# Kernel tuning notes

Measured on AMD Instinct MI355X. Metric: run time of the kernel, lower is better.

The kernel has to match this reference:

```python
import jax, jax.numpy as jnp
import numpy as np

B, T, C, H = 8, 2048, 1024, 64


def setup_inputs() -> dict:
    key = jax.random.key(0)
    kx, kq, kk, kv = jax.random.split(key, 4)
    sc = 1.0 / np.sqrt(C)
    return {
        "x": jax.random.normal(kx, (B, T, C), dtype=jnp.float32),
        "Wq": jax.random.normal(kq, (C, H), dtype=jnp.float32) * sc,
        "Wk": jax.random.normal(kk, (C, H), dtype=jnp.float32) * sc,
        "Wv": jax.random.normal(kv, (C, H), dtype=jnp.float32) * sc,
    }


def reference(x, Wq, Wk, Wv):
    # Projections: Linear(C, head_size, bias=False) == x @ W
    q = jnp.einsum("btc,ch->bth", x, Wq)
    k = jnp.einsum("btc,ch->bth", x, Wk)
    v = jnp.einsum("btc,ch->bth", x, Wv)
    head_size = q.shape[-1]
    scale = head_size ** -0.5
    # scores: [B, T, T]
    scores = jnp.einsum("bqh,bkh->bqk", q, k) * scale
    # causal mask (tril==0 -> -inf)
    causal = jnp.tril(jnp.ones((scores.shape[1], scores.shape[2]), dtype=bool))
    scores = jnp.where(causal, scores, -jnp.inf)
    w = jax.nn.softmax(scores, axis=-1)
    # dropout_rate=0.0 -> identity
    out = jnp.einsum("bqk,bkh->bqh", w, v)
    return out
```

## Files before the change

### kernel.cpp

```cpp
#include <hip/hip_runtime.h>
#include <hip/hip_bf16.h>
#include <cstdint>
#include <cstddef>

typedef short bf16x8 __attribute__((ext_vector_type(8)));
typedef float f32x4 __attribute__((ext_vector_type(4)));

#define BN 8
#define TN 2048
#define CN 1024
#define HN 64

__device__ __forceinline__ unsigned short f2bf(float f) {
    unsigned int u = __float_as_uint(f);
    u += 0x7fffu + ((u >> 16) & 1u);
    return (unsigned short)(u >> 16);
}

__device__ __forceinline__ int pk2(float lo, float hi) {
    float2 t; t.x = lo; t.y = hi;
    __hip_bfloat162 h = __float22bfloat162_rn(t);
    return *reinterpret_cast<int*>(&h);
}

__device__ __forceinline__ void gload_lds16(const unsigned short* gsrc, void* ldst) {
    __builtin_amdgcn_global_load_lds(
        (const __attribute__((address_space(1))) unsigned int*)gsrc,
        (__attribute__((address_space(3))) unsigned int*)ldst,
        16, 0, 0);
}

__global__ __launch_bounds__(256) void wconv_kernel(const float* __restrict__ Wq,
                                                    const float* __restrict__ Wk,
                                                    const float* __restrict__ Wv,
                                                    unsigned short* __restrict__ Wp) {
    int idx = blockIdx.x * 256 + threadIdx.x;
    int n = idx >> 10;
    int c = idx & 1023;
    int m = n >> 6;
    int h = n & 63;
    const float* W = (m == 0) ? Wq : ((m == 1) ? Wk : Wv);
    float v = W[c * 64 + h];
    if (m == 0) v *= 0.18033688011112042f;
    const int tile = n >> 4, lq = n & 15;
    const int kk = c >> 5, lg = (c >> 3) & 3, e = c & 7;
    Wp[(size_t)(((tile * 32 + kk) * 64 + lg * 16 + lq) * 8 + e)] = f2bf(v);
}

__global__ __launch_bounds__(512) void proj_kernel(const float* __restrict__ X,
                                                   const unsigned short* __restrict__ Wp,
                                                   unsigned short* __restrict__ Qs,
                                                   unsigned short* __restrict__ Kp,
                                                   unsigned short* __restrict__ Vp) {
    __shared__ short Xs[2][64 * 64];
    __shared__ short Wsh[2][6144];

    const int tid = threadIdx.x;
    const int w   = tid >> 6;
    const int l   = tid & 63;
    const int lq  = l & 15;
    const int lg  = l >> 4;
    const int mr   = w >> 1;
    const int nsub = w & 1;
    const int bid = blockIdx.x;
    const int mtile = bid & 255;
    const int nh    = bid >> 8;
    const int rowbase = mtile * 64;

    const int xrow = tid >> 3;
    const int xcol = (tid & 7) * 8;
    const float* xsrc = X + (size_t)(rowbase + xrow) * CN + xcol;
    const int xdst = xrow * 128 + (((xcol * 2)) ^ ((xrow & 7) << 4));

    const unsigned short* wsrc0 = Wp + (size_t)((nh * 6 + (w >> 1)) * 32 + (w & 1)) * 512 + l * 8;
    const int wdstb0 = (w * 512) * 2;
    const unsigned short* wsrc1 = Wp + (size_t)((nh * 6 + 4 + (w >> 1)) * 32 + (w & 1)) * 512 + l * 8;
    const int wdstb1 = (4096 + w * 512) * 2;

    const int arow = mr * 16 + lq;
    int aaddr[2];
    #pragma unroll
    for (int kkL = 0; kkL < 2; ++kkL)
        aaddr[kkL] = arow * 128 + (((kkL * 64 + lg * 16)) ^ ((arow & 7) << 4));
    int baddr[2][3];
    #pragma unroll
    for (int kkL = 0; kkL < 2; ++kkL)
        #pragma unroll
        for (int jj = 0; jj < 3; ++jj)
            baddr[kkL][jj] = (((nsub * 3 + jj) * 2 + kkL) * 512 + l * 8) * 2;

    const f32x4 zero4 = {0.f, 0.f, 0.f, 0.f};
    f32x4 acc[3] = {zero4, zero4, zero4};

    {
        gload_lds16(wsrc0, (char*)Wsh[0] + wdstb0);
        if (tid < 256) gload_lds16(wsrc1, (char*)Wsh[0] + wdstb1);
        float4 xa = *(const float4*)(xsrc);
        float4 xb = *(const float4*)(xsrc + 4);
        int4 xc;
        xc.x = pk2(xa.x, xa.y); xc.y = pk2(xa.z, xa.w);
        xc.z = pk2(xb.x, xb.y); xc.w = pk2(xb.z, xb.w);
        *(int4*)((char*)Xs[0] + xdst) = xc;
        __syncthreads();
    }

    for (int s = 0; s < 16; ++s) {
        const int cur = s & 1;
        const int nxt = cur ^ 1;
        const bool more = (s + 1) < 16;
        float4 xa, xb;
        if (more) {
            xa = *(const float4*)(xsrc + (s + 1) * 64);
            xb = *(const float4*)(xsrc + (s + 1) * 64 + 4);
            gload_lds16(wsrc0 + (s + 1) * 1024, (char*)Wsh[nxt] + wdstb0);
            if (tid < 256) gload_lds16(wsrc1 + (s + 1) * 1024, (char*)Wsh[nxt] + wdstb1);
        }
        #pragma unroll
        for (int kkL = 0; kkL < 2; ++kkL) {
            bf16x8 a  = *(const bf16x8*)((char*)Xs[cur] + aaddr[kkL]);
            bf16x8 b0 = *(const bf16x8*)((char*)Wsh[cur] + baddr[kkL][0]);
            bf16x8 b1 = *(const bf16x8*)((char*)Wsh[cur] + baddr[kkL][1]);
            bf16x8 b2 = *(const bf16x8*)((char*)Wsh[cur] + baddr[kkL][2]);
            acc[0] = __builtin_amdgcn_mfma_f32_16x16x32_bf16(a, b0, acc[0], 0, 0, 0);
            acc[1] = __builtin_amdgcn_mfma_f32_16x16x32_bf16(a, b1, acc[1], 0, 0, 0);
            acc[2] = __builtin_amdgcn_mfma_f32_16x16x32_bf16(a, b2, acc[2], 0, 0, 0);
        }
        if (more) {
            int4 xc;
            xc.x = pk2(xa.x, xa.y); xc.y = pk2(xa.z, xa.w);
            xc.z = pk2(xb.x, xb.y); xc.w = pk2(xb.z, xb.w);
            *(int4*)((char*)Xs[nxt] + xdst) = xc;
        }
        __syncthreads();
    }

    #pragma unroll
    for (int jj = 0; jj < 3; ++jj) {
        const int col = nh * 96 + nsub * 48 + jj * 16 + lq;
        const int mtx = col >> 6;
        const int h   = col & 63;
        #pragma unroll
        for (int i = 0; i < 4; ++i) {
            const int g = rowbase + mr * 16 + 4 * lg + i;
            const unsigned short val = f2bf(acc[jj][i]);
            const int b = g >> 11, tloc = g & 2047;
            const int kt = tloc >> 5;
            if (mtx == 0) {
                Qs[(size_t)g * 64 + h] = val;
            } else if (mtx == 1) {
                const int fa = (tloc >> 4) & 1, lqk = tloc & 15;
                const int ks = h >> 5, lgk = (h >> 3) & 3, e = h & 7;
                Kp[(size_t)(b * 64 + kt) * 2048 + (fa * 2 + ks) * 512 +
                   (lgk * 16 + lqk) * 8 + e] = val;
            } else {
                const int tt = tloc & 31;
                const int lgv = (tt & 15) >> 2;
                const int e = (tt < 16) ? (tt & 3) : 4 + (tt & 3);
                const int nf = h >> 4, lqv = h & 15;
                Vp[(size_t)(b * 64 + kt) * 2048 + nf * 512 +
                   (lgv * 16 + lqv) * 8 + e] = val;
            }
        }
    }
}

__global__ __launch_bounds__(256) void attn_kernel(const unsigned short* __restrict__ Qs,
                                                   const unsigned short* __restrict__ Kp,
                                                   const unsigned short* __restrict__ Vp,
                                                   float* __restrict__ Out) {
    __shared__ float lm[4][16];
    __shared__ float ll[4][16];
    __shared__ float facc[4][1024];

    const int tid = threadIdx.x;
    const int w  = tid >> 6;
    const int l  = tid & 63;
    const int lq = l & 15;
    const int lg = l >> 4;
    const int bid = blockIdx.x;
    const int qt = 127 - (bid >> 3);
    const int b  = bid & 7;
    const int q0 = qt * 16;
    const int nt = (qt >> 1) + 1;

    const unsigned short* Qb = Qs + (size_t)b * TN * 64;
    const unsigned short* KVbase_k = Kp + (size_t)b * 64 * 2048 + (size_t)l * 8;
    const unsigned short* KVbase_v = Vp + (size_t)b * 64 * 2048 + (size_t)l * 8;

    const f32x4 zero4 = {0.f, 0.f, 0.f, 0.f};

    bf16x8 qa0 = *(const bf16x8*)(Qb + (size_t)(q0 + lq) * 64 + lg * 8);
    bf16x8 qa1 = *(const bf16x8*)(Qb + (size_t)(q0 + lq) * 64 + 32 + lg * 8);

    f32x4 acc[4] = {zero4, zero4, zero4, zero4};
    float mrow = -1e30f;
    float lrow = 0.f;

    bf16x8 Kc[4], Vc[4], Kn[4], Vn[4];
    int kt = w;
    if (kt < nt) {
        const size_t tb = (size_t)kt * 2048;
        #pragma unroll
        for (int i = 0; i < 4; ++i) {
            Kc[i] = *(const bf16x8*)(KVbase_k + tb + i * 512);
            Vc[i] = *(const bf16x8*)(KVbase_v + tb + i * 512);
        }
    }

    for (; kt < nt; kt += 4) {
        const int ktn = kt + 4;
        if (ktn < nt) {
            const size_t tb = (size_t)ktn * 2048;
            #pragma unroll
            for (int i = 0; i < 4; ++i) {
                Kn[i] = *(const bf16x8*)(KVbase_k + tb + i * 512);
                Vn[i] = *(const bf16x8*)(KVbase_v + tb + i * 512);
            }
        }

        const int key0 = kt * 32;
        f32x4 s[2];
        s[0] = __builtin_amdgcn_mfma_f32_16x16x32_bf16(Kc[0], qa0, zero4, 0, 0, 0);
        s[0] = __builtin_amdgcn_mfma_f32_16x16x32_bf16(Kc[1], qa1, s[0], 0, 0, 0);
        s[1] = __builtin_amdgcn_mfma_f32_16x16x32_bf16(Kc[2], qa0, zero4, 0, 0, 0);
        s[1] = __builtin_amdgcn_mfma_f32_16x16x32_bf16(Kc[3], qa1, s[1], 0, 0, 0);

        if (kt == nt - 1) {
            const int q = q0 + lq;
            #pragma unroll
            for (int fa = 0; fa < 2; ++fa)
                #pragma unroll
                for (int r = 0; r < 4; ++r) {
                    const int key = key0 + fa * 16 + 4 * lg + r;
                    if (key > q) s[fa][r] = -1e30f;
                }
        }

        float m1 = fmaxf(fmaxf(s[0][0], s[0][1]), s[0][2]);
        float m2 = fmaxf(fmaxf(s[0][3], s[1][0]), s[1][1]);
        float m3 = fmaxf(fmaxf(s[1][2], s[1][3]), m1);
        float tm = fmaxf(m2, m3);
        tm = fmaxf(tm, __shfl_xor(tm, 16));
        tm = fmaxf(tm, __shfl_xor(tm, 32));

        if (!__all(tm <= mrow + 8.0f)) {
            const float mnew = fmaxf(mrow, tm);
            const float cc = __builtin_amdgcn_exp2f(mrow - mnew);
            lrow *= cc;
            float cb[4];
            #pragma unroll
            for (int i = 0; i < 4; ++i) cb[i] = __shfl(cc, 4 * lg + i);
            #pragma unroll
            for (int nf = 0; nf < 4; ++nf)
                #pragma unroll
                for (int i = 0; i < 4; ++i) acc[nf][i] *= cb[i];
            mrow = mnew;
        }

        float p[2][4];
        float psum = 0.f;
        #pragma unroll
        for (int fa = 0; fa < 2; ++fa)
            #pragma unroll
            for (int r = 0; r < 4; ++r) {
                p[fa][r] = __builtin_amdgcn_exp2f(s[fa][r] - mrow);
                psum += p[fa][r];
            }
        psum += __shfl_xor(psum, 16);
        psum += __shfl_xor(psum, 32);
        lrow += psum;

        bf16x8 pa;
        pa[0] = (short)f2bf(p[0][0]); pa[1] = (short)f2bf(p[0][1]);
        pa[2] = (short)f2bf(p[0][2]); pa[3] = (short)f2bf(p[0][3]);
        pa[4] = (short)f2bf(p[1][0]); pa[5] = (short)f2bf(p[1][1]);
        pa[6] = (short)f2bf(p[1][2]); pa[7] = (short)f2bf(p[1][3]);

        acc[0] = __builtin_amdgcn_mfma_f32_16x16x32_bf16(pa, Vc[0], acc[0], 0, 0, 0);
        acc[1] = __builtin_amdgcn_mfma_f32_16x16x32_bf16(pa, Vc[1], acc[1], 0, 0, 0);
        acc[2] = __builtin_amdgcn_mfma_f32_16x16x32_bf16(pa, Vc[2], acc[2], 0, 0, 0);
        acc[3] = __builtin_amdgcn_mfma_f32_16x16x32_bf16(pa, Vc[3], acc[3], 0, 0, 0);

        #pragma unroll
        for (int i = 0; i < 4; ++i) { Kc[i] = Kn[i]; Vc[i] = Vn[i]; }
    }

    if (lg == 0) {
        lm[w][lq] = mrow;
        ll[w][lq] = lrow;
    }
    #pragma unroll
    for (int nf = 0; nf < 4; ++nf)
        #pragma unroll
        for (int i = 0; i < 4; ++i)
            facc[w][(4 * lg + i) * 64 + nf * 16 + lq] = acc[nf][i];

    __syncthreads();

    #pragma unroll
    for (int ii = 0; ii < 4; ++ii) {
        const int e = tid + ii * 256;
        const int q = e >> 6;
        const int h = e & 63;
        const float M = fmaxf(fmaxf(lm[0][q], lm[1][q]),
                              fmaxf(lm[2][q], lm[3][q]));
        float L = 0.f, O = 0.f;
        #pragma unroll
        for (int c = 0; c < 4; ++c) {
            const float wgt = __builtin_amdgcn_exp2f(lm[c][q] - M);
            L += wgt * ll[c][q];
            O += wgt * facc[c][q * 64 + h];
        }
        Out[((size_t)b * TN + q0 + q) * 64 + h] = O / L;
    }
}

extern "C" void kernel_launch(void* const* d_in, const int* in_sizes, int n_in,
                              void* d_out, int out_size, void* d_ws, size_t ws_size,
                              hipStream_t stream) {
    const float* X  = (const float*)d_in[0];
    const float* Wq = (const float*)d_in[1];
    const float* Wk = (const float*)d_in[2];
    const float* Wv = (const float*)d_in[3];
    float* Out = (float*)d_out;

    char* ws = (char*)d_ws;
    unsigned short* Wp = (unsigned short*)(ws);
    unsigned short* Qs = (unsigned short*)(ws + (512u << 10));
    unsigned short* Kp = Qs + (size_t)16384 * 64;
    unsigned short* Vp = Kp + (size_t)16384 * 64;

    hipLaunchKernelGGL(wconv_kernel, dim3(768), dim3(256), 0, stream, Wq, Wk, Wv, Wp);
    hipLaunchKernelGGL(proj_kernel,  dim3(512), dim3(512), 0, stream, X, Wp, Qs, Kp, Vp);
    hipLaunchKernelGGL(attn_kernel,  dim3(1024), dim3(256), 0, stream, Qs, Kp, Vp, Out);
}
```

Before: 43.25 us.

## Switch projection GEMM to 32x32x16 MFMA with six-wave 32x32 tiles

Measured after the change: 43.38 us. No clear change (+0.3%).

```diff
diff --git a/kernel.cpp b/kernel.cpp
--- a/kernel.cpp
+++ b/kernel.cpp
@@ -5,6 +5,7 @@
 
 typedef short bf16x8 __attribute__((ext_vector_type(8)));
 typedef float f32x4 __attribute__((ext_vector_type(4)));
+typedef float f32x16 __attribute__((ext_vector_type(16)));
 
 #define BN 8
 #define TN 2048
@@ -42,65 +43,77 @@
     const float* W = (m == 0) ? Wq : ((m == 1) ? Wk : Wv);
     float v = W[c * 64 + h];
     if (m == 0) v *= 0.18033688011112042f;
-    const int tile = n >> 4, lq = n & 15;
-    const int kk = c >> 5, lg = (c >> 3) & 3, e = c & 7;
-    Wp[(size_t)(((tile * 32 + kk) * 64 + lg * 16 + lq) * 8 + e)] = f2bf(v);
-}
-
-__global__ __launch_bounds__(512) void proj_kernel(const float* __restrict__ X,
+    const int tc = n >> 5, col = n & 31;
+    const int kk16 = c >> 4, khalf = (c >> 3) & 1, e = c & 7;
+    const int l = col + 32 * khalf;
+    Wp[(size_t)(((tc * 64 + kk16) * 64 + l) * 8 + e)] = f2bf(v);
+}
+
+__global__ __launch_bounds__(384) void proj_kernel(const float* __restrict__ X,
                                                    const unsigned short* __restrict__ Wp,
                                                    unsigned short* __restrict__ Qs,
                                                    unsigned short* __restrict__ Kp,
                                                    unsigned short* __restrict__ Vp) {
-    __shared__ short Xs[2][64 * 64];
+    __shared__ short Xs[2][4096];
     __shared__ short Wsh[2][6144];
 
     const int tid = threadIdx.x;
     const int w   = tid >> 6;
     const int l   = tid & 63;
-    const int lq  = l & 15;
-    const int lg  = l >> 4;
-    const int mr   = w >> 1;
-    const int nsub = w & 1;
+    const int m   = w / 3;
+    const int ntL = w % 3;
     const int bid = blockIdx.x;
     const int mtile = bid & 255;
     const int nh    = bid >> 8;
     const int rowbase = mtile * 64;
 
-    const int xrow = tid >> 3;
-    const int xcol = (tid & 7) * 8;
-    const float* xsrc = X + (size_t)(rowbase + xrow) * CN + xcol;
-    const int xdst = xrow * 128 + (((xcol * 2)) ^ ((xrow & 7) << 4));
-
-    const unsigned short* wsrc0 = Wp + (size_t)((nh * 6 + (w >> 1)) * 32 + (w & 1)) * 512 + l * 8;
-    const int wdstb0 = (w * 512) * 2;
-    const unsigned short* wsrc1 = Wp + (size_t)((nh * 6 + 4 + (w >> 1)) * 32 + (w & 1)) * 512 + l * 8;
-    const int wdstb1 = (4096 + w * 512) * 2;
-
-    const int arow = mr * 16 + lq;
-    int aaddr[2];
-    #pragma unroll
-    for (int kkL = 0; kkL < 2; ++kkL)
-        aaddr[kkL] = arow * 128 + (((kkL * 64 + lg * 16)) ^ ((arow & 7) << 4));
-    int baddr[2][3];
-    #pragma unroll
-    for (int kkL = 0; kkL < 2; ++kkL)
-        #pragma unroll
-        for (int jj = 0; jj < 3; ++jj)
-            baddr[kkL][jj] = (((nsub * 3 + jj) * 2 + kkL) * 512 + l * 8) * 2;
-
-    const f32x4 zero4 = {0.f, 0.f, 0.f, 0.f};
-    f32x4 acc[3] = {zero4, zero4, zero4};
+    const int r0 = tid >> 3;
+    const float* xsrc0 = X + (size_t)(rowbase + r0) * CN + (tid & 7) * 8;
+    const int xdst0 = r0 * 128 + (((tid & 7) * 16) ^ ((r0 & 7) << 4));
+    const int u1 = tid + 384;
+    const int r1 = u1 >> 3;
+    const float* xsrc1 = X + (size_t)(rowbase + r1) * CN + (u1 & 7) * 8;
+    const int xdst1 = r1 * 128 + (((u1 & 7) * 16) ^ ((r1 & 7) << 4));
+    const bool st2 = (tid < 128);
+
+    const unsigned short* wsrc[2];
+    int wdst[2];
+    #pragma unroll
+    for (int i = 0; i < 2; ++i) {
+        const int c = 2 * w + i;
+        const int tcL = c >> 2, kkL = c & 3;
+        wsrc[i] = Wp + (size_t)((nh * 3 + tcL) * 64 + kkL) * 512 + l * 8;
+        wdst[i] = c * 1024;
+    }
+
+    int aaddr[4], baddr[4];
+    #pragma unroll
+    for (int j = 0; j < 4; ++j) {
+        aaddr[j] = (m * 32 + (l & 31)) * 128 +
+                   ((j * 32 + (l >> 5) * 16) ^ ((l & 7) << 4));
+        baddr[j] = (ntL * 4 + j) * 1024 + l * 16;
+    }
+
+    f32x16 acc = {0.f, 0.f, 0.f, 0.f, 0.f, 0.f, 0.f, 0.f,
+                  0.f, 0.f, 0.f, 0.f, 0.f, 0.f, 0.f, 0.f};
 
     {
-        gload_lds16(wsrc0, (char*)Wsh[0] + wdstb0);
-        if (tid < 256) gload_lds16(wsrc1, (char*)Wsh[0] + wdstb1);
-        float4 xa = *(const float4*)(xsrc);
-        float4 xb = *(const float4*)(xsrc + 4);
+        gload_lds16(wsrc[0], (char*)Wsh[0] + wdst[0]);
+        gload_lds16(wsrc[1], (char*)Wsh[0] + wdst[1]);
+        float4 xa = *(const float4*)(xsrc0);
+        float4 xb = *(const float4*)(xsrc0 + 4);
         int4 xc;
         xc.x = pk2(xa.x, xa.y); xc.y = pk2(xa.z, xa.w);
         xc.z = pk2(xb.x, xb.y); xc.w = pk2(xb.z, xb.w);
-        *(int4*)((char*)Xs[0] + xdst) = xc;
+        *(int4*)((char*)Xs[0] + xdst0) = xc;
+        if (st2) {
+            float4 ya = *(const float4*)(xsrc1);
+            float4 yb = *(const float4*)(xsrc1 + 4);
+            int4 yc;
+            yc.x = pk2(ya.x, ya.y); yc.y = pk2(ya.z, ya.w);
+            yc.z = pk2(yb.x, yb.y); yc.w = pk2(yb.z, yb.w);
+            *(int4*)((char*)Xs[0] + xdst1) = yc;
+        }
         __syncthreads();
     }
 
@@ -108,58 +121,62 @@
         const int cur = s & 1;
         const int nxt = cur ^ 1;
         const bool more = (s + 1) < 16;
-        float4 xa, xb;
+        float4 xa, xb, ya, yb;
         if (more) {
-            xa = *(const float4*)(xsrc + (s + 1) * 64);
-            xb = *(const float4*)(xsrc + (s + 1) * 64 + 4);
-            gload_lds16(wsrc0 + (s + 1) * 1024, (char*)Wsh[nxt] + wdstb0);
-            if (tid < 256) gload_lds16(wsrc1 + (s + 1) * 1024, (char*)Wsh[nxt] + wdstb1);
-        }
-        #pragma unroll
-        for (int kkL = 0; kkL < 2; ++kkL) {
-            bf16x8 a  = *(const bf16x8*)((char*)Xs[cur] + aaddr[kkL]);
-            bf16x8 b0 = *(const bf16x8*)((char*)Wsh[cur] + baddr[kkL][0]);
-            bf16x8 b1 = *(const bf16x8*)((char*)Wsh[cur] + baddr[kkL][1]);
-            bf16x8 b2 = *(const bf16x8*)((char*)Wsh[cur] + baddr[kkL][2]);
-            acc[0] = __builtin_amdgcn_mfma_f32_16x16x32_bf16(a, b0, acc[0], 0, 0, 0);
-            acc[1] = __builtin_amdgcn_mfma_f32_16x16x32_bf16(a, b1, acc[1], 0, 0, 0);
-            acc[2] = __builtin_amdgcn_mfma_f32_16x16x32_bf16(a, b2, acc[2], 0, 0, 0);
+            gload_lds16(wsrc[0] + (s + 1) * 2048, (char*)Wsh[nxt] + wdst[0]);
+            gload_lds16(wsrc[1] + (s + 1) * 2048, (char*)Wsh[nxt] + wdst[1]);
+            xa = *(const float4*)(xsrc0 + (s + 1) * 64);
+            xb = *(const float4*)(xsrc0 + (s + 1) * 64 + 4);
+            if (st2) {
+                ya = *(const float4*)(xsrc1 + (s + 1) * 64);
+                yb = *(const float4*)(xsrc1 + (s + 1) * 64 + 4);
+            }
+        }
+        #pragma unroll
+        for (int j = 0; j < 4; ++j) {
+            bf16x8 a = *(const bf16x8*)((char*)Xs[cur] + aaddr[j]);
+            bf16x8 b = *(const bf16x8*)((char*)Wsh[cur] + baddr[j]);
+            acc = __builtin_amdgcn_mfma_f32_32x32x16_bf16(a, b, acc, 0, 0, 0);
         }
         if (more) {
             int4 xc;
             xc.x = pk2(xa.x, xa.y); xc.y = pk2(xa.z, xa.w);
             xc.z = pk2(xb.x, xb.y); xc.w = pk2(xb.z, xb.w);
-            *(int4*)((char*)Xs[nxt] + xdst) = xc;
+            *(int4*)((char*)Xs[nxt] + xdst0) = xc;
+            if (st2) {
+                int4 yc;
+                yc.x = pk2(ya.x, ya.y); yc.y = pk2(ya.z, ya.w);
+                yc.z = pk2(yb.x, yb.y); yc.w = pk2(yb.z, yb.w);
+                *(int4*)((char*)Xs[nxt] + xdst1) = yc;
+            }
         }
         __syncthreads();
     }
 
-    #pragma unroll
-    for (int jj = 0; jj < 3; ++jj) {
-        const int col = nh * 96 + nsub * 48 + jj * 16 + lq;
-        const int mtx = col >> 6;
-        const int h   = col & 63;
-        #pragma unroll
-        for (int i = 0; i < 4; ++i) {
-            const int g = rowbase + mr * 16 + 4 * lg + i;
-            const unsigned short val = f2bf(acc[jj][i]);
-            const int b = g >> 11, tloc = g & 2047;
-            const int kt = tloc >> 5;
-            if (mtx == 0) {
-                Qs[(size_t)g * 64 + h] = val;
-            } else if (mtx == 1) {
-                const int fa = (tloc >> 4) & 1, lqk = tloc & 15;
-                const int ks = h >> 5, lgk = (h >> 3) & 3, e = h & 7;
-                Kp[(size_t)(b * 64 + kt) * 2048 + (fa * 2 + ks) * 512 +
-                   (lgk * 16 + lqk) * 8 + e] = val;
-            } else {
-                const int tt = tloc & 31;
-                const int lgv = (tt & 15) >> 2;
-                const int e = (tt < 16) ? (tt & 3) : 4 + (tt & 3);
-                const int nf = h >> 4, lqv = h & 15;
-                Vp[(size_t)(b * 64 + kt) * 2048 + nf * 512 +
-                   (lgv * 16 + lqv) * 8 + e] = val;
-            }
+    const int col = nh * 96 + ntL * 32 + (l & 31);
+    const int mtx = col >> 6;
+    const int h   = col & 63;
+    #pragma unroll
+    for (int r16 = 0; r16 < 16; ++r16) {
+        const int row32 = (r16 & 3) + 8 * (r16 >> 2) + 4 * (l >> 5);
+        const int g = rowbase + m * 32 + row32;
+        const unsigned short val = f2bf(acc[r16]);
+        const int b = g >> 11, tloc = g & 2047;
+        const int kt = tloc >> 5;
+        if (mtx == 0) {
+            Qs[(size_t)g * 64 + h] = val;
+        } else if (mtx == 1) {
+            const int fa = (tloc >> 4) & 1, lqk = tloc & 15;
+            const int ks = h >> 5, lgk = (h >> 3) & 3, e = h & 7;
+            Kp[(size_t)(b * 64 + kt) * 2048 + (fa * 2 + ks) * 512 +
+               (lgk * 16 + lqk) * 8 + e] = val;
+        } else {
+            const int tt = tloc & 31;
+            const int lgv = (tt & 15) >> 2;
+            const int e = (tt < 16) ? (tt & 3) : 4 + (tt & 3);
+            const int nf = h >> 4, lqv = h & 15;
+            Vp[(size_t)(b * 64 + kt) * 2048 + nf * 512 +
+               (lgv * 16 + lqv) * 8 + e] = val;
         }
     }
 }
@@ -331,6 +348,6 @@
     unsigned short* Vp = Kp + (size_t)16384 * 64;
 
     hipLaunchKernelGGL(wconv_kernel, dim3(768), dim3(256), 0, stream, Wq, Wk, Wv, Wp);
-    hipLaunchKernelGGL(proj_kernel,  dim3(512), dim3(512), 0, stream, X, Wp, Qs, Kp, Vp);
+    hipLaunchKernelGGL(proj_kernel,  dim3(512), dim3(384), 0, stream, X, Wp, Qs, Kp, Vp);
     hipLaunchKernelGGL(attn_kernel,  dim3(1024), dim3(256), 0, stream, Qs, Kp, Vp, Out);
 }
```
